# Kernel optimization log

Hardware: AMD Instinct MI355X
Metric: run time of the kernel (lower is better)

The kernel has to match this reference:

```python
import jax, jax.numpy as jnp
import numpy as np

N = 2048
D_T = 256; D_F = 256
E_T = 32; E_F = 32; E_C = 128
C = 5; Q = 512


def setup_inputs() -> dict:
    key = jax.random.key(0)
    ks = jax.random.split(key, 12)
    # full graph minus self-loops, row-major (matches dense_to_sparse ordering)
    r, c = np.meshgrid(np.arange(N), np.arange(N), indexing='ij')
    m = r != c
    edge_index = jnp.asarray(np.stack([r[m], c[m]]), dtype=jnp.int32)  # [2, N*(N-1)]
    E = edge_index.shape[1]
    s = 0.02
    return {
        'time_features': jax.random.normal(ks[0], (N, D_T), jnp.float32),
        'edge_index': edge_index,
        'time_edge_weight': jax.random.uniform(ks[1], (E,), jnp.float32),
        'freq_features': jax.random.normal(ks[2], (N, D_F), jnp.float32),
        'freq_edge_weight': jax.random.uniform(ks[3], (E,), jnp.float32),
        'labels': jax.random.randint(ks[4], (N,), 0, C, jnp.int32),
        'num_classes': C,
        'query_size': Q,
        'Wt': jax.random.normal(ks[5], (D_T, E_T), jnp.float32) * s,
        'bt': jnp.zeros((E_T,), jnp.float32),
        'Wf': jax.random.normal(ks[6], (D_F, E_F), jnp.float32) * s,
        'bf': jnp.zeros((E_F,), jnp.float32),
        'Wc': jax.random.normal(ks[7], (E_T + E_F + C, E_C), jnp.float32) * s,
        'bc': jnp.zeros((E_C,), jnp.float32),
        'Wo': jax.random.normal(ks[8], (E_C, C), jnp.float32) * s,
        'bo': jnp.zeros((C,), jnp.float32),
    }


def _gcn(x, A, W, b):
    # torch_geometric GCNConv: D^{-1/2}(A + I)D^{-1/2} (X W) + b
    n = A.shape[0]
    Ah = A + jnp.eye(n, dtype=A.dtype)
    deg = Ah.sum(axis=1)
    dis = jnp.where(deg > 0, jax.lax.rsqrt(deg), 0.0)
    return (dis[:, None] * Ah * dis[None, :]) @ (x @ W) + b


def reference(time_features, edge_index, time_edge_weight, freq_features,
              freq_edge_weight, labels, num_classes, query_size,
              Wt, bt, Wf, bf, Wc, bc, Wo, bo):
    n = time_features.shape[0]
    lrelu = lambda z: jax.nn.leaky_relu(z, 0.01)

    def dense_adj(w):  # A[dst, src] = w
        return jnp.zeros((n, n), w.dtype).at[edge_index[1], edge_index[0]].add(w)

    te = lrelu(_gcn(time_features, dense_adj(time_edge_weight), Wt, bt))
    fe = lrelu(_gcn(freq_features, dense_adj(freq_edge_weight), Wf, bf))

    # to_one_hot: one_hot[:n - query_size, labels] = 1 -> support rows get 1 in
    # every column that appears anywhere in `labels`
    cols = jnp.zeros((num_classes,), te.dtype).at[labels].set(1.0)
    rowmask = (jnp.arange(n) < (n - query_size)).astype(te.dtype)
    one_hot = rowmask[:, None] * cols[None, :]

    feats = jnp.concatenate([te, fe, one_hot], axis=-1)  # [n, E_T+E_F+C]

    # graph_construction (no_grad in original): 1 / (L1 distance over the
    # non-one-hot dims + 1e-5), zero diagonal
    fd = jax.lax.stop_gradient(feats[:, : feats.shape[1] - num_classes])
    dist = jnp.sum(jnp.abs(fd[:, None, :] - fd[None, :, :]), axis=-1)  # [n, n]
    Aw = (1.0 / (dist + 1e-5)) * (1.0 - jnp.eye(n, dtype=feats.dtype))

    emb = lrelu(_gcn(feats, Aw, Wc, bc))
    return emb @ Wo + bo
```

## Files before the change

kernel.cpp:

```cpp
#include <hip/hip_runtime.h>
#include <hip/hip_bf16.h>

#define N 2048
#define NM1 2047
#define DT 256
#define ET 32
#define EC 128
#define NC 5
#define FS 80
#define FD 69
#define KC_ET 16
#define KC_EC 16

typedef __hip_bfloat16 bf16;

__global__ __launch_bounds__(256) void k_deg_label_xw(const float* __restrict__ tw,
                                                      const float* __restrict__ fw,
                                                      const int* __restrict__ labels,
                                                      const float* __restrict__ Xt,
                                                      const float* __restrict__ Wt,
                                                      const float* __restrict__ Xf,
                                                      const float* __restrict__ Wf,
                                                      float* __restrict__ degT,
                                                      float* __restrict__ degF,
                                                      float* __restrict__ cols,
                                                      float* __restrict__ Yt,
                                                      float* __restrict__ Yf){
    int b = blockIdx.x;
    int t = threadIdx.x;
    if (b < 512){
        int p = (b & 7)*256 + t;
        if (p >= NM1) return;
        int s0 = (b >> 3)*32;
        float lowT=0.f, highT=0.f, lowF=0.f, highF=0.f;
        #pragma unroll 8
        for (int r = 0; r < 32; ++r){
            int s = s0 + r;
            float vt = tw[(size_t)s*NM1 + p];
            float vf = fw[(size_t)s*NM1 + p];
            if (s <= p){ highT += vt; highF += vf; }
            else       { lowT  += vt; lowF  += vf; }
        }
        atomicAdd(&degT[p],   lowT);
        atomicAdd(&degF[p],   lowF);
        atomicAdd(&degT[p+1], highT);
        atomicAdd(&degF[p+1], highF);
        return;
    }
    if (b == 512){
        __shared__ float lc[NC];
        if (t < NC) lc[t] = 0.f;
        __syncthreads();
        for (int i = t; i < N; i += 256){
            int l = labels[i];
            if (l >= 0 && l < NC) lc[l] = 1.f;
        }
        __syncthreads();
        if (t < NC) cols[t] = lc[t];
        return;
    }
    int idx = b - 513;
    const float* X = (idx & 256) ? Xf : Xt;
    const float* W = (idx & 256) ? Wf : Wt;
    float*       Y = (idx & 256) ? Yf : Yt;
    __shared__ float Ws[DT*ET];
    __shared__ float Xs[8*DT];
    for (int j = t; j < DT*ET; j += 256) Ws[j] = W[j];
    int i0 = (idx & 255)*8;
    for (int j = t; j < 8*DT; j += 256) Xs[j] = X[(size_t)i0*DT + j];
    __syncthreads();
    int r = t >> 5, f = t & 31;
    const float* xr = Xs + r*DT;
    float acc = 0.f;
    #pragma unroll 8
    for (int d = 0; d < DT; ++d) acc += xr[d]*Ws[d*ET+f];
    Y[(size_t)(i0+r)*ET+f] = acc;
}

__global__ __launch_bounds__(256) void k_agg_et(const float* __restrict__ tw,
                                                const float* __restrict__ fw,
                                                const float* __restrict__ Yt,
                                                const float* __restrict__ Yf,
                                                const float* __restrict__ degT,
                                                const float* __restrict__ degF,
                                                float* __restrict__ Pt,
                                                float* __restrict__ Pf){
    __shared__ float Ast[64*68];
    __shared__ float Asf[64*68];
    __shared__ float Zst[64*ET];
    __shared__ float Zsf[64*ET];
    int t = threadIdx.x;
    int i0 = blockIdx.x*64;
    int kc = blockIdx.y;
    int k0 = kc*128;
    int g  = t >> 7;
    int tt = t & 127;
    int ig = tt >> 3, fg = tt & 7;
    int r0 = ig*4, c0 = fg*4;
    const float* As = g ? Asf : Ast;
    const float* Zs = g ? Zsf : Zst;
    float acc[4][4];
    #pragma unroll
    for (int u=0;u<4;++u)
        #pragma unroll
        for (int v=0;v<4;++v) acc[u][v]=0.f;

    for (int kt = 0; kt < 2; ++kt){
        int kb = k0 + kt*64;
        #pragma unroll
        for (int e = 0; e < 16; ++e){
            int id = t + e*256;
            int k_l = id >> 6, i_l = id & 63;
            int k = kb + k_l;
            int gi = i0 + i_l;
            float vt, vf;
            if (gi == k){ vt = 0.f; vf = 0.f; }
            else {
                size_t base = (size_t)k*NM1 + gi - (gi > k ? 1 : 0);
                vt = tw[base]; vf = fw[base];
            }
            Ast[k_l*68 + i_l] = vt;
            Asf[k_l*68 + i_l] = vf;
        }
        #pragma unroll
        for (int e = 0; e < 2; ++e){
            int id = t + e*256;
            int row = id >> 3;
            int c4  = (id & 7)*4;
            float rdT = rsqrtf(1.f + degT[kb+row]);
            float rdF = rsqrtf(1.f + degF[kb+row]);
            float4 yt = *(const float4*)&Yt[(size_t)(kb+row)*ET + c4];
            float4 yf = *(const float4*)&Yf[(size_t)(kb+row)*ET + c4];
            yt.x*=rdT; yt.y*=rdT; yt.z*=rdT; yt.w*=rdT;
            yf.x*=rdF; yf.y*=rdF; yf.z*=rdF; yf.w*=rdF;
            *(float4*)&Zst[row*ET + c4] = yt;
            *(float4*)&Zsf[row*ET + c4] = yf;
        }
        __syncthreads();
        for (int k = 0; k < 64; ++k){
            float4 a = *(const float4*)&As[k*68 + r0];
            float4 z = *(const float4*)&Zs[k*ET + c0];
            const float* ap = (const float*)&a;
            const float* zp = (const float*)&z;
            #pragma unroll
            for (int u = 0; u < 4; ++u)
                #pragma unroll
                for (int v = 0; v < 4; ++v)
                    acc[u][v] += ap[u]*zp[v];
        }
        __syncthreads();
    }
    float* P = g ? Pf : Pt;
    #pragma unroll
    for (int u = 0; u < 4; ++u){
        size_t ii = (size_t)(i0 + r0 + u);
        float4 o;
        float* po = (float*)&o;
        #pragma unroll
        for (int v = 0; v < 4; ++v) po[v]=acc[u][v];
        *(float4*)&P[(size_t)kc*(N*ET) + ii*ET + c0] = o;
    }
}

__global__ __launch_bounds__(256) void k_feats_epi(const float* __restrict__ Pt,
                                                   const float* __restrict__ Pf,
                                                   const float* __restrict__ Yt,
                                                   const float* __restrict__ Yf,
                                                   const float* __restrict__ degT,
                                                   const float* __restrict__ degF,
                                                   const float* __restrict__ bt,
                                                   const float* __restrict__ bfv,
                                                   const float* __restrict__ cols,
                                                   const int* __restrict__ qsize,
                                                   float* __restrict__ feats){
    int idx = blockIdx.x*256 + threadIdx.x;
    int i = idx >> 6;
    int f = idx & 63;
    float s, rd, b;
    if (f < ET){
        rd = rsqrtf(1.f + degT[i]);
        s = rd*Yt[(size_t)i*ET + f];
        #pragma unroll
        for (int kc = 0; kc < KC_ET; ++kc) s += Pt[(size_t)kc*(N*ET) + (size_t)i*ET + f];
        b = bt[f];
    } else {
        int g = f - ET;
        rd = rsqrtf(1.f + degF[i]);
        s = rd*Yf[(size_t)i*ET + g];
        #pragma unroll
        for (int kc = 0; kc < KC_ET; ++kc) s += Pf[(size_t)kc*(N*ET) + (size_t)i*ET + g];
        b = bfv[g];
    }
    float v = rd*s + b;
    feats[(size_t)i*FS + f] = v > 0.f ? v : 0.01f*v;
    if (f < NC){
        int nsup = N - qsize[0];
        feats[(size_t)i*FS + 2*ET + f] = (i < nsup) ? cols[f] : 0.f;
    }
}

__global__ __launch_bounds__(256) void k_build_aw(const float* __restrict__ feats,
                                                  float* __restrict__ Aw,
                                                  float* __restrict__ dsum){
    __shared__ float fiT[64*68];
    __shared__ float fjT[64*68];
    int t = threadIdx.x;
    int i0 = blockIdx.x*64, j0 = blockIdx.y*64;
    {
        int row = t >> 2;
        int cb  = (t & 3)*16;
        const float4* si = (const float4*)(feats + (size_t)(i0+row)*FS + cb);
        const float4* sj = (const float4*)(feats + (size_t)(j0+row)*FS + cb);
        #pragma unroll
        for (int s = 0; s < 4; ++s){
            float4 v = si[s];
            float4 w = sj[s];
            int c = cb + s*4;
            fiT[(c+0)*68+row]=v.x; fiT[(c+1)*68+row]=v.y; fiT[(c+2)*68+row]=v.z; fiT[(c+3)*68+row]=v.w;
            fjT[(c+0)*68+row]=w.x; fjT[(c+1)*68+row]=w.y; fjT[(c+2)*68+row]=w.z; fjT[(c+3)*68+row]=w.w;
        }
    }
    __syncthreads();
    int tx = t & 15, ty = t >> 4;
    float acc[4][4];
    #pragma unroll
    for (int u=0;u<4;++u)
        #pragma unroll
        for (int v=0;v<4;++v) acc[u][v]=0.f;
    for (int d = 0; d < 64; ++d){
        float4 a4 = *(const float4*)&fiT[d*68 + ty*4];
        float4 b4 = *(const float4*)&fjT[d*68 + tx*4];
        const float* ap = (const float*)&a4;
        const float* bp = (const float*)&b4;
        #pragma unroll
        for (int u = 0; u < 4; ++u)
            #pragma unroll
            for (int v = 0; v < 4; ++v)
                acc[u][v] += fabsf(ap[u]-bp[v]);
    }
    #pragma unroll
    for (int u = 0; u < 4; ++u){
        int gi = i0 + ty*4 + u;
        float4 o;
        float* po = (float*)&o;
        #pragma unroll
        for (int v = 0; v < 4; ++v){
            int gj = j0 + tx*4 + v;
            po[v] = (gi==gj) ? 1.0f : 1.0f/(acc[u][v] + 1e-5f);
        }
        *(float4*)&Aw[(size_t)gi*N + j0 + tx*4] = o;
        float rs = (po[0]+po[1]) + (po[2]+po[3]);
        rs += __shfl_xor(rs, 1);
        rs += __shfl_xor(rs, 2);
        rs += __shfl_xor(rs, 4);
        rs += __shfl_xor(rs, 8);
        if (tx == 0) atomicAdd(&dsum[gi], rs);
    }
}

__global__ __launch_bounds__(256) void k_featswc(const float* __restrict__ feats,
                                                 const float* __restrict__ Wc,
                                                 const float* __restrict__ dsum,
                                                 float* __restrict__ Zc){
    __shared__ float Wcs[FD*EC];
    __shared__ float fr[8][FD+3];
    int t = threadIdx.x;
    for (int idx = t; idx < FD*EC; idx += 256) Wcs[idx] = Wc[idx];
    int i0 = blockIdx.x*8;
    for (int idx = t; idx < 8*FD; idx += 256){
        int r = idx / FD;
        int c = idx - r*FD;
        fr[r][c] = feats[(size_t)(i0+r)*FS + c];
    }
    __syncthreads();
    int f  = t & 127;
    int rh = t >> 7;
    for (int rr = 0; rr < 4; ++rr){
        int r = rh*4 + rr;
        float acc = 0.f;
        #pragma unroll
        for (int d = 0; d < FD; ++d) acc += fr[r][d]*Wcs[d*EC+f];
        int i = i0 + r;
        Zc[(size_t)i*EC + f] = rsqrtf(dsum[i])*acc;
    }
}

__global__ __launch_bounds__(256) void k_agg_ec(const float* __restrict__ Aw,
                                                const float* __restrict__ Zc,
                                                float* __restrict__ Pe){
    __shared__ float As[64*68];
    __shared__ float Zs[64*128];
    int t = threadIdx.x;
    int i0 = blockIdx.x*64;
    int kc = blockIdx.y;
    int k0 = kc*128;
    int rg = t >> 4;
    int cg = t & 15;
    int r0 = rg*4;
    int ca = cg*4, cb = 64 + cg*4;
    float acc[4][8];
    #pragma unroll
    for (int u=0;u<4;++u)
        #pragma unroll
        for (int v=0;v<8;++v) acc[u][v]=0.f;

    for (int kt = 0; kt < 2; ++kt){
        int kb = k0 + kt*64;
        #pragma unroll
        for (int e = 0; e < 4; ++e){
            int id = t + e*256;
            int k_l = id >> 4;
            int i4  = (id & 15)*4;
            *(float4*)&As[k_l*68 + i4] = *(const float4*)&Aw[(size_t)(kb+k_l)*N + i0 + i4];
        }
        #pragma unroll
        for (int e = 0; e < 8; ++e){
            int id = t + e*256;
            int k_l = id >> 5;
            int c4  = (id & 31)*4;
            *(float4*)&Zs[k_l*128 + c4] = *(const float4*)&Zc[(size_t)(kb+k_l)*EC + c4];
        }
        __syncthreads();
        for (int k = 0; k < 64; ++k){
            float4 a  = *(const float4*)&As[k*68 + r0];
            float4 z0 = *(const float4*)&Zs[k*128 + ca];
            float4 z1 = *(const float4*)&Zs[k*128 + cb];
            float a4[4] = {a.x,a.y,a.z,a.w};
            float zl[4] = {z0.x,z0.y,z0.z,z0.w};
            float zh[4] = {z1.x,z1.y,z1.z,z1.w};
            #pragma unroll
            for (int u = 0; u < 4; ++u){
                #pragma unroll
                for (int v = 0; v < 4; ++v){
                    acc[u][v]   += a4[u]*zl[v];
                    acc[u][v+4] += a4[u]*zh[v];
                }
            }
        }
        __syncthreads();
    }
    #pragma unroll
    for (int u = 0; u < 4; ++u){
        size_t ii = (size_t)(i0 + r0 + u);
        float4 o0, o1;
        float* p0 = (float*)&o0; float* p1 = (float*)&o1;
        #pragma unroll
        for (int v = 0; v < 4; ++v){ p0[v]=acc[u][v]; p1[v]=acc[u][v+4]; }
        *(float4*)&Pe[(size_t)kc*(N*EC) + ii*EC + ca] = o0;
        *(float4*)&Pe[(size_t)kc*(N*EC) + ii*EC + cb] = o1;
    }
}

__global__ __launch_bounds__(256) void k_embfinal(const float* __restrict__ Pe,
                                                  const float* __restrict__ dsum,
                                                  const float* __restrict__ bc,
                                                  const float* __restrict__ Wo,
                                                  const float* __restrict__ bo,
                                                  float* __restrict__ out){
    __shared__ float vs[2][EC];
    __shared__ float Wos[EC*NC];
    __shared__ float bos[NC];
    int t = threadIdx.x;
    for (int idx = t; idx < EC*NC; idx += 256) Wos[idx] = Wo[idx];
    if (t < NC) bos[t] = bo[t];
    int rr = t >> 7, f = t & 127;
    int i = blockIdx.x*2 + rr;
    size_t idx = (size_t)i*EC + f;
    float s = 0.f;
    #pragma unroll
    for (int kc = 0; kc < KC_EC; ++kc) s += Pe[(size_t)kc*(N*EC) + idx];
    float v = rsqrtf(dsum[i])*s + bc[f];
    vs[rr][f] = v > 0.f ? v : 0.01f*v;
    __syncthreads();
    if (t < 2*NC){
        int r = t / NC;
        int c = t - r*NC;
        float a = bos[c];
        #pragma unroll 8
        for (int f2 = 0; f2 < EC; ++f2) a += vs[r][f2]*Wos[f2*NC+c];
        out[(size_t)(blockIdx.x*2 + r)*NC + c] = a;
    }
}

extern "C" void kernel_launch(void* const* d_in, const int* in_sizes, int n_in,
                              void* d_out, int out_size, void* d_ws, size_t ws_size,
                              hipStream_t stream) {
    const float* time_features = (const float*)d_in[0];
    const float* tw            = (const float*)d_in[2];
    const float* freq_features = (const float*)d_in[3];
    const float* fw            = (const float*)d_in[4];
    const int*   labels        = (const int*)d_in[5];
    const int*   qsize         = (const int*)d_in[7];
    const float* Wt  = (const float*)d_in[8];
    const float* bt  = (const float*)d_in[9];
    const float* Wf  = (const float*)d_in[10];
    const float* bfv = (const float*)d_in[11];
    const float* Wc  = (const float*)d_in[12];
    const float* bc  = (const float*)d_in[13];
    const float* Wo  = (const float*)d_in[14];
    const float* bo  = (const float*)d_in[15];
    float* out = (float*)d_out;

    float* ws    = (float*)d_ws;
    float* Yt    = ws;
    float* Yf    = Yt + (size_t)N*ET;
    float* Zc    = Yf + (size_t)N*ET;
    float* degT  = Zc + (size_t)N*EC;
    float* degF  = degT + N;
    float* dsum  = degF + N;
    float* colsb = dsum + N;
    float* feats = colsb + 8;
    float* Aw    = feats + (size_t)N*FS;
    float* Pt    = Aw + (size_t)N*N;
    float* Pf    = Pt + (size_t)KC_ET*N*ET;
    float* Pe    = Pf + (size_t)KC_ET*N*ET;

    hipMemsetAsync(degT, 0, 3*N*sizeof(float), stream);
    k_deg_label_xw<<<1025, 256, 0, stream>>>(tw, fw, labels,
                                             time_features, Wt, freq_features, Wf,
                                             degT, degF, colsb, Yt, Yf);
    k_agg_et<<<dim3(N/64, KC_ET), 256, 0, stream>>>(tw, fw, Yt, Yf, degT, degF, Pt, Pf);
    k_feats_epi<<<(N*64)/256, 256, 0, stream>>>(Pt, Pf, Yt, Yf, degT, degF,
                                                bt, bfv, colsb, qsize, feats);
    k_build_aw<<<dim3(N/64, N/64), 256, 0, stream>>>(feats, Aw, dsum);
    k_featswc<<<N/8, 256, 0, stream>>>(feats, Wc, dsum, Zc);
    k_agg_ec<<<dim3(N/64, KC_EC), 256, 0, stream>>>(Aw, Zc, Pe);
    k_embfinal<<<N/2, 256, 0, stream>>>(Pe, dsum, bc, Wo, bo, out);
}
```

Before: 206.7 us.

## Replace split-K partial buffers with atomic accumulation and fuse epilogues

The split-K GCN aggregation kernels now atomically add their partial sums straight into feats and emb instead of writing per-chunk partial buffers. This removes the separate k_feats_epi kernel and the 16-way partial reductions in k_embfinal. The leaky-ReLU moves to the consumers (build_aw, featswc) because the atomic sums are not activated when written, and the workspace is reordered so one memset zeroes the accumulators. It adds float atomics, which make summation order nondeterministic and could contend on the same addresses.

```diff
diff --git a/kernel.cpp b/kernel.cpp
--- a/kernel.cpp
+++ b/kernel.cpp
@@ -13,6 +13,8 @@
 #define KC_EC 16
 
 typedef __hip_bfloat16 bf16;
+
+__device__ __forceinline__ float lrelu(float v){ return v > 0.f ? v : 0.01f*v; }
 
 __global__ __launch_bounds__(256) void k_deg_label_xw(const float* __restrict__ tw,
                                                       const float* __restrict__ fw,
@@ -83,8 +85,11 @@
                                                 const float* __restrict__ Yf,
                                                 const float* __restrict__ degT,
                                                 const float* __restrict__ degF,
-                                                float* __restrict__ Pt,
-                                                float* __restrict__ Pf){
+                                                const float* __restrict__ bt,
+                                                const float* __restrict__ bfv,
+                                                const float* __restrict__ cols,
+                                                const int* __restrict__ qsize,
+                                                float* __restrict__ feats){
     __shared__ float Ast[64*68];
     __shared__ float Asf[64*68];
     __shared__ float Zst[64*ET];
@@ -150,52 +155,30 @@
         }
         __syncthreads();
     }
-    float* P = g ? Pf : Pt;
+    const float* deg  = g ? degF : degT;
+    const float* Y    = g ? Yf   : Yt;
+    const float* bias = g ? bfv  : bt;
+    int fOff = g ? ET : 0;
     #pragma unroll
     for (int u = 0; u < 4; ++u){
-        size_t ii = (size_t)(i0 + r0 + u);
-        float4 o;
-        float* po = (float*)&o;
-        #pragma unroll
-        for (int v = 0; v < 4; ++v) po[v]=acc[u][v];
-        *(float4*)&P[(size_t)kc*(N*ET) + ii*ET + c0] = o;
-    }
-}
-
-__global__ __launch_bounds__(256) void k_feats_epi(const float* __restrict__ Pt,
-                                                   const float* __restrict__ Pf,
-                                                   const float* __restrict__ Yt,
-                                                   const float* __restrict__ Yf,
-                                                   const float* __restrict__ degT,
-                                                   const float* __restrict__ degF,
-                                                   const float* __restrict__ bt,
-                                                   const float* __restrict__ bfv,
-                                                   const float* __restrict__ cols,
-                                                   const int* __restrict__ qsize,
-                                                   float* __restrict__ feats){
-    int idx = blockIdx.x*256 + threadIdx.x;
-    int i = idx >> 6;
-    int f = idx & 63;
-    float s, rd, b;
-    if (f < ET){
-        rd = rsqrtf(1.f + degT[i]);
-        s = rd*Yt[(size_t)i*ET + f];
-        #pragma unroll
-        for (int kc = 0; kc < KC_ET; ++kc) s += Pt[(size_t)kc*(N*ET) + (size_t)i*ET + f];
-        b = bt[f];
-    } else {
-        int g = f - ET;
-        rd = rsqrtf(1.f + degF[i]);
-        s = rd*Yf[(size_t)i*ET + g];
-        #pragma unroll
-        for (int kc = 0; kc < KC_ET; ++kc) s += Pf[(size_t)kc*(N*ET) + (size_t)i*ET + g];
-        b = bfv[g];
-    }
-    float v = rd*s + b;
-    feats[(size_t)i*FS + f] = v > 0.f ? v : 0.01f*v;
-    if (f < NC){
+        int gi = i0 + r0 + u;
+        float rdv = rsqrtf(1.f + deg[gi]);
+        #pragma unroll
+        for (int v = 0; v < 4; ++v){
+            float val = rdv*acc[u][v];
+            if (kc == 0)
+                val += rdv*rdv*Y[(size_t)gi*ET + c0 + v] + bias[c0 + v];
+            atomicAdd(&feats[(size_t)gi*FS + fOff + c0 + v], val);
+        }
+    }
+    if (kc == 0){
         int nsup = N - qsize[0];
-        feats[(size_t)i*FS + 2*ET + f] = (i < nsup) ? cols[f] : 0.f;
+        for (int id = t; id < 64*NC; id += 256){
+            int row = id / NC;
+            int c   = id - row*NC;
+            int gi  = i0 + row;
+            feats[(size_t)gi*FS + 2*ET + c] = (gi < nsup) ? cols[c] : 0.f;
+        }
     }
 }
 
@@ -216,8 +199,10 @@
             float4 v = si[s];
             float4 w = sj[s];
             int c = cb + s*4;
-            fiT[(c+0)*68+row]=v.x; fiT[(c+1)*68+row]=v.y; fiT[(c+2)*68+row]=v.z; fiT[(c+3)*68+row]=v.w;
-            fjT[(c+0)*68+row]=w.x; fjT[(c+1)*68+row]=w.y; fjT[(c+2)*68+row]=w.z; fjT[(c+3)*68+row]=w.w;
+            fiT[(c+0)*68+row]=lrelu(v.x); fiT[(c+1)*68+row]=lrelu(v.y);
+            fiT[(c+2)*68+row]=lrelu(v.z); fiT[(c+3)*68+row]=lrelu(v.w);
+            fjT[(c+0)*68+row]=lrelu(w.x); fjT[(c+1)*68+row]=lrelu(w.y);
+            fjT[(c+2)*68+row]=lrelu(w.z); fjT[(c+3)*68+row]=lrelu(w.w);
         }
     }
     __syncthreads();
@@ -270,7 +255,7 @@
     for (int idx = t; idx < 8*FD; idx += 256){
         int r = idx / FD;
         int c = idx - r*FD;
-        fr[r][c] = feats[(size_t)(i0+r)*FS + c];
+        fr[r][c] = lrelu(feats[(size_t)(i0+r)*FS + c]);
     }
     __syncthreads();
     int f  = t & 127;
@@ -287,7 +272,7 @@
 
 __global__ __launch_bounds__(256) void k_agg_ec(const float* __restrict__ Aw,
                                                 const float* __restrict__ Zc,
-                                                float* __restrict__ Pe){
+                                                float* __restrict__ emb){
     __shared__ float As[64*68];
     __shared__ float Zs[64*128];
     int t = threadIdx.x;
@@ -342,16 +327,15 @@
     #pragma unroll
     for (int u = 0; u < 4; ++u){
         size_t ii = (size_t)(i0 + r0 + u);
-        float4 o0, o1;
-        float* p0 = (float*)&o0; float* p1 = (float*)&o1;
-        #pragma unroll
-        for (int v = 0; v < 4; ++v){ p0[v]=acc[u][v]; p1[v]=acc[u][v+4]; }
-        *(float4*)&Pe[(size_t)kc*(N*EC) + ii*EC + ca] = o0;
-        *(float4*)&Pe[(size_t)kc*(N*EC) + ii*EC + cb] = o1;
-    }
-}
-
-__global__ __launch_bounds__(256) void k_embfinal(const float* __restrict__ Pe,
+        #pragma unroll
+        for (int v = 0; v < 4; ++v){
+            atomicAdd(&emb[ii*EC + ca + v], acc[u][v]);
+            atomicAdd(&emb[ii*EC + cb + v], acc[u][v+4]);
+        }
+    }
+}
+
+__global__ __launch_bounds__(256) void k_embfinal(const float* __restrict__ emb,
                                                   const float* __restrict__ dsum,
                                                   const float* __restrict__ bc,
                                                   const float* __restrict__ Wo,
@@ -365,10 +349,7 @@
     if (t < NC) bos[t] = bo[t];
     int rr = t >> 7, f = t & 127;
     int i = blockIdx.x*2 + rr;
-    size_t idx = (size_t)i*EC + f;
-    float s = 0.f;
-    #pragma unroll
-    for (int kc = 0; kc < KC_EC; ++kc) s += Pe[(size_t)kc*(N*EC) + idx];
+    float s = emb[(size_t)i*EC + f];
     float v = rsqrtf(dsum[i])*s + bc[f];
     vs[rr][f] = v > 0.f ? v : 0.01f*v;
     __syncthreads();
@@ -402,28 +383,26 @@
     float* out = (float*)d_out;
 
     float* ws    = (float*)d_ws;
-    float* Yt    = ws;
+    float* degT  = ws;
+    float* degF  = degT + N;
+    float* dsum  = degF + N;
+    float* feats = dsum + N;
+    float* emb   = feats + (size_t)N*FS;
+    float* colsb = emb + (size_t)N*EC;
+    float* Yt    = colsb + 8;
     float* Yf    = Yt + (size_t)N*ET;
     float* Zc    = Yf + (size_t)N*ET;
-    float* degT  = Zc + (size_t)N*EC;
-    float* degF  = degT + N;
-    float* dsum  = degF + N;
-    float* colsb = dsum + N;
-    float* feats = colsb + 8;
-    float* Aw    = feats + (size_t)N*FS;
-    float* Pt    = Aw + (size_t)N*N;
-    float* Pf    = Pt + (size_t)KC_ET*N*ET;
-    float* Pe    = Pf + (size_t)KC_ET*N*ET;
-
-    hipMemsetAsync(degT, 0, 3*N*sizeof(float), stream);
+    float* Aw    = Zc + (size_t)N*EC;
+
+    size_t zeroBytes = (size_t)(3*N + N*FS + N*EC)*sizeof(float);
+    hipMemsetAsync(degT, 0, zeroBytes, stream);
     k_deg_label_xw<<<1025, 256, 0, stream>>>(tw, fw, labels,
                                              time_features, Wt, freq_features, Wf,
                                              degT, degF, colsb, Yt, Yf);
-    k_agg_et<<<dim3(N/64, KC_ET), 256, 0, stream>>>(tw, fw, Yt, Yf, degT, degF, Pt, Pf);
-    k_feats_epi<<<(N*64)/256, 256, 0, stream>>>(Pt, Pf, Yt, Yf, degT, degF,
-                                                bt, bfv, colsb, qsize, feats);
+    k_agg_et<<<dim3(N/64, KC_ET), 256, 0, stream>>>(tw, fw, Yt, Yf, degT, degF,
+                                                    bt, bfv, colsb, qsize, feats);
     k_build_aw<<<dim3(N/64, N/64), 256, 0, stream>>>(feats, Aw, dsum);
     k_featswc<<<N/8, 256, 0, stream>>>(feats, Wc, dsum, Zc);
-    k_agg_ec<<<dim3(N/64, KC_EC), 256, 0, stream>>>(Aw, Zc, Pe);
-    k_embfinal<<<N/2, 256, 0, stream>>>(Pe, dsum, bc, Wo, bo, out);
-}
+    k_agg_ec<<<dim3(N/64, KC_EC), 256, 0, stream>>>(Aw, Zc, emb);
+    k_embfinal<<<N/2, 256, 0, stream>>>(emb, dsum, bc, Wo, bo, out);
+}
```

After: 275.3 us. +33.2%, slower.
